# Kernel tuning notes

Measured on AMD Instinct MI355X. Metric: run time of the kernel, lower is better.

The kernel has to match this reference:

```python
import jax, jax.numpy as jnp
import numpy as np

TOKENS = 8192
HIDDEN = 4096
EPS = 1e-6
FP8_MAX = 448.0  # max finite value of float8_e4m3fn


def setup_inputs() -> dict:
    key = jax.random.key(0)
    k1, k2, k3 = jax.random.split(key, 3)
    x = jax.random.normal(k1, (TOKENS, HIDDEN), jnp.float32)
    # RMSNorm gains near 1
    norm_w = 1.0 + 0.1 * jax.random.normal(k2, (4, HIDDEN), jnp.float32)
    Ws = 0.02 * jax.random.normal(k3, (3, HIDDEN, HIDDEN), jnp.float32)
    # static per-tensor weight scales (amax / fp8_max)
    w_scales = jnp.max(jnp.abs(Ws), axis=(1, 2)) / FP8_MAX
    return {"x": x, "norm_w": norm_w, "Ws": Ws, "w_scales": w_scales}


def _rmsnorm(x, w):
    var = jnp.mean(x * x, axis=-1, keepdims=True)
    return x * jax.lax.rsqrt(var + EPS) * w


def _quant_dequant_fp8(v, s):
    # quantize to e4m3 with scale s, then dequantize (emulated fp8 GEMM inputs)
    q = (v / s).astype(jnp.float8_e4m3fn)
    return q.astype(jnp.float32) * s


def _fp8_linear(y, W, w_scale):
    # dynamic per-token activation scale
    a_scale = jnp.maximum(jnp.max(jnp.abs(y), axis=-1, keepdims=True) / FP8_MAX, 1e-12)
    yq = _quant_dequant_fp8(y, a_scale)           # [T, H]
    Wq = _quant_dequant_fp8(W, w_scale)           # [H, H]
    return yq @ Wq.T                              # torch.nn.Linear convention


def reference(x, norm_w, Ws, w_scales):
    x = jax.nn.relu(x)
    resid = x
    y = _rmsnorm(x, norm_w[0])                    # plain RMSNorm
    for i in range(3):
        h = _fp8_linear(y, Ws[i], w_scales[i])    # FP8 GEMM
        resid = h + resid                         # fused add + RMSNorm
        y = _rmsnorm(resid, norm_w[i + 1])
    return y
```

## Files before the change

### kernel.cpp

```cpp
#include <hip/hip_runtime.h>
#include <stdint.h>

#define TOKENS 8192
#define HIDDEN 4096
constexpr float EPS = 1e-6f;
constexpr float FP8_MAX = 448.0f;

using f32x4  = __attribute__((ext_vector_type(4))) float;
using f32x16 = __attribute__((ext_vector_type(16))) float;
using i32x4  = __attribute__((ext_vector_type(4))) int;
using i32x8  = __attribute__((ext_vector_type(8))) int;

typedef __attribute__((address_space(3))) uint32_t lds_u32_t;
typedef const __attribute__((address_space(1))) uint32_t glb_u32_t;

__device__ inline uint32_t pack_fp8x4(float a, float b, float c, float d) {
    int w = 0;
    w = __builtin_amdgcn_cvt_pk_fp8_f32(a, b, w, false);
    w = __builtin_amdgcn_cvt_pk_fp8_f32(c, d, w, true);
    return (uint32_t)w;
}

__device__ inline float block_sum(float v, float* sh, int tid) {
#pragma unroll
    for (int o = 32; o > 0; o >>= 1) v += __shfl_xor(v, o, 64);
    if ((tid & 63) == 0) sh[tid >> 6] = v;
    __syncthreads();
    return sh[0] + sh[1] + sh[2] + sh[3];
}
__device__ inline float block_max(float v, float* sh, int tid) {
#pragma unroll
    for (int o = 32; o > 0; o >>= 1) v = fmaxf(v, __shfl_xor(v, o, 64));
    if ((tid & 63) == 0) sh[tid >> 6] = v;
    __syncthreads();
    return fmaxf(fmaxf(sh[0], sh[1]), fmaxf(sh[2], sh[3]));
}

__launch_bounds__(256)
__global__ void quant_weights(const float* __restrict__ Ws,
                              const float* __restrict__ w_scales,
                              uint8_t* __restrict__ Wq) {
    size_t idx = ((size_t)blockIdx.x * 256 + threadIdx.x) * 8;
    int tensor = (int)(idx / ((size_t)HIDDEN * HIDDEN));
    float inv = 1.0f / w_scales[tensor];
    const float4* src = (const float4*)(Ws + idx);
    float4 v0 = src[0], v1 = src[1];
    uint2 out;
    out.x = pack_fp8x4(v0.x * inv, v0.y * inv, v0.z * inv, v0.w * inv);
    out.y = pack_fp8x4(v1.x * inv, v1.y * inv, v1.z * inv, v1.w * inv);
    *(uint2*)(Wq + idx) = out;
}

__launch_bounds__(256)
__global__ void relu_rms_quant(const float* __restrict__ x,
                               const float* __restrict__ nw,
                               float* __restrict__ resid,
                               uint8_t* __restrict__ yq,
                               float* __restrict__ ascale) {
    __shared__ float sh1[4], sh2[4];
    const int row = blockIdx.x, tid = threadIdx.x;
    const float* xr = x + (size_t)row * HIDDEN;
    float* rr = resid + (size_t)row * HIDDEN;

    float4 v[4];
    float ss = 0.f;
#pragma unroll
    for (int c = 0; c < 4; ++c) {
        float4 t = *(const float4*)(xr + c * 1024 + tid * 4);
        t.x = fmaxf(t.x, 0.f); t.y = fmaxf(t.y, 0.f);
        t.z = fmaxf(t.z, 0.f); t.w = fmaxf(t.w, 0.f);
        v[c] = t;
        ss += t.x * t.x + t.y * t.y + t.z * t.z + t.w * t.w;
        *(float4*)(rr + c * 1024 + tid * 4) = t;
    }
    ss = block_sum(ss, sh1, tid);
    float rstd = 1.0f / sqrtf(ss * (1.0f / HIDDEN) + EPS);

    float4 y[4];
    float amax = 0.f;
#pragma unroll
    for (int c = 0; c < 4; ++c) {
        float4 w = *(const float4*)(nw + c * 1024 + tid * 4);
        y[c].x = v[c].x * rstd * w.x; amax = fmaxf(amax, fabsf(y[c].x));
        y[c].y = v[c].y * rstd * w.y; amax = fmaxf(amax, fabsf(y[c].y));
        y[c].z = v[c].z * rstd * w.z; amax = fmaxf(amax, fabsf(y[c].z));
        y[c].w = v[c].w * rstd * w.w; amax = fmaxf(amax, fabsf(y[c].w));
    }
    amax = block_max(amax, sh2, tid);
    float s = fmaxf(amax / FP8_MAX, 1e-12f);
    if (tid == 0) ascale[row] = s;
    float inv = 1.0f / s;
#pragma unroll
    for (int c = 0; c < 4; ++c) {
        uint32_t p = pack_fp8x4(y[c].x * inv, y[c].y * inv, y[c].z * inv, y[c].w * inv);
        *(uint32_t*)(yq + (size_t)row * HIDDEN + c * 1024 + tid * 4) = p;
    }
}

__launch_bounds__(256)
__global__ void rms_quant(const float* __restrict__ resid,
                          const float* __restrict__ nw,
                          uint8_t* __restrict__ yq,
                          float* __restrict__ ascale) {
    __shared__ float sh1[4], sh2[4];
    const int row = blockIdx.x, tid = threadIdx.x;
    const float* rr = resid + (size_t)row * HIDDEN;

    float4 v[4];
    float ss = 0.f;
#pragma unroll
    for (int c = 0; c < 4; ++c) {
        float4 t = *(const float4*)(rr + c * 1024 + tid * 4);
        v[c] = t;
        ss += t.x * t.x + t.y * t.y + t.z * t.z + t.w * t.w;
    }
    ss = block_sum(ss, sh1, tid);
    float rstd = 1.0f / sqrtf(ss * (1.0f / HIDDEN) + EPS);

    float4 y[4];
    float amax = 0.f;
#pragma unroll
    for (int c = 0; c < 4; ++c) {
        float4 w = *(const float4*)(nw + c * 1024 + tid * 4);
        y[c].x = v[c].x * rstd * w.x; amax = fmaxf(amax, fabsf(y[c].x));
        y[c].y = v[c].y * rstd * w.y; amax = fmaxf(amax, fabsf(y[c].y));
        y[c].z = v[c].z * rstd * w.z; amax = fmaxf(amax, fabsf(y[c].z));
        y[c].w = v[c].w * rstd * w.w; amax = fmaxf(amax, fabsf(y[c].w));
    }
    amax = block_max(amax, sh2, tid);
    float s = fmaxf(amax / FP8_MAX, 1e-12f);
    if (tid == 0) ascale[row] = s;
    float inv = 1.0f / s;
#pragma unroll
    for (int c = 0; c < 4; ++c) {
        uint32_t p = pack_fp8x4(y[c].x * inv, y[c].y * inv, y[c].z * inv, y[c].w * inv);
        *(uint32_t*)(yq + (size_t)row * HIDDEN + c * 1024 + tid * 4) = p;
    }
}

__launch_bounds__(256)
__global__ void rms_final(const float* __restrict__ resid,
                          const float* __restrict__ nw,
                          float* __restrict__ out) {
    __shared__ float sh1[4];
    const int row = blockIdx.x, tid = threadIdx.x;
    const float* rr = resid + (size_t)row * HIDDEN;

    float4 v[4];
    float ss = 0.f;
#pragma unroll
    for (int c = 0; c < 4; ++c) {
        float4 t = *(const float4*)(rr + c * 1024 + tid * 4);
        v[c] = t;
        ss += t.x * t.x + t.y * t.y + t.z * t.z + t.w * t.w;
    }
    ss = block_sum(ss, sh1, tid);
    float rstd = 1.0f / sqrtf(ss * (1.0f / HIDDEN) + EPS);

#pragma unroll
    for (int c = 0; c < 4; ++c) {
        float4 w = *(const float4*)(nw + c * 1024 + tid * 4);
        float4 o;
        o.x = v[c].x * rstd * w.x;
        o.y = v[c].y * rstd * w.y;
        o.z = v[c].z * rstd * w.z;
        o.w = v[c].w * rstd * w.w;
        *(float4*)(out + (size_t)row * HIDDEN + c * 1024 + tid * 4) = o;
    }
}

#define BM 128
#define BN 128
#define BK 64

__launch_bounds__(256)
__global__ void gemm_fp8(const uint8_t* __restrict__ Aq,
                         const uint8_t* __restrict__ Bq,
                         const float* __restrict__ ascale,
                         const float* __restrict__ wscale_p,
                         float* __restrict__ resid) {
    __shared__ __align__(16) uint8_t sA[BM * BK];
    __shared__ __align__(16) uint8_t sB[BN * BK];
    __shared__ float s_as[BM];

    const int tid = threadIdx.x;
    int bid = blockIdx.x;
    bid = (bid & 7) * 256 + (bid >> 3);
    const int nbn = HIDDEN / BN;
    const int bm = bid / nbn, bn = bid % nbn;
    const int brow = bm * BM, bcol = bn * BN;

    const int wave = tid >> 6, lane = tid & 63;
    const int wm = wave >> 1, wn = wave & 1;
    const int lr = lane & 31;
    const int lh = lane >> 5;

    if (tid < BM) s_as[tid] = ascale[brow + tid];

    f32x16 acc[2][2] = {};

    const uint8_t* aSrc = Aq + (size_t)brow * HIDDEN;
    const uint8_t* bSrc = Bq + (size_t)bcol * HIDDEN;

    const int r_st = tid >> 2;
    const int g_st = tid & 3;
    const int gsrc = g_st ^ ((r_st >> 1) & 3);
    const size_t off0 = (size_t)r_st * HIDDEN + gsrc * 16;
    const size_t off1 = (size_t)(r_st + 64) * HIDDEN + gsrc * 16;
    uint8_t* ldsA0 = &sA[wave * 1024];
    uint8_t* ldsA1 = &sA[4096 + wave * 1024];
    uint8_t* ldsB0 = &sB[wave * 1024];
    uint8_t* ldsB1 = &sB[4096 + wave * 1024];

    int offA[2][2], offB[2][2];
#pragma unroll
    for (int m = 0; m < 2; ++m) {
        int ra = wm * 64 + m * 32 + lr;
        int sa_ = (ra >> 1) & 3;
        offA[m][0] = ra * 64 + ((2 * lh + 0) ^ sa_) * 16;
        offA[m][1] = ra * 64 + ((2 * lh + 1) ^ sa_) * 16;
        int rb = wn * 64 + m * 32 + lr;
        int sb_ = (rb >> 1) & 3;
        offB[m][0] = rb * 64 + ((2 * lh + 0) ^ sb_) * 16;
        offB[m][1] = rb * 64 + ((2 * lh + 1) ^ sb_) * 16;
    }

    const int UNIT = 0x7F7F7F7F;

    for (int k0 = 0; k0 < HIDDEN; k0 += BK) {
        __syncthreads();
        __builtin_amdgcn_global_load_lds((glb_u32_t*)(aSrc + off0 + k0),
                                         (lds_u32_t*)ldsA0, 16, 0, 0);
        __builtin_amdgcn_global_load_lds((glb_u32_t*)(aSrc + off1 + k0),
                                         (lds_u32_t*)ldsA1, 16, 0, 0);
        __builtin_amdgcn_global_load_lds((glb_u32_t*)(bSrc + off0 + k0),
                                         (lds_u32_t*)ldsB0, 16, 0, 0);
        __builtin_amdgcn_global_load_lds((glb_u32_t*)(bSrc + off1 + k0),
                                         (lds_u32_t*)ldsB1, 16, 0, 0);
        __syncthreads();

        i32x8 a[2], b[2];
#pragma unroll
        for (int m = 0; m < 2; ++m) {
            i32x4 lo = *(const i32x4*)&sA[offA[m][0]];
            i32x4 hi = *(const i32x4*)&sA[offA[m][1]];
            a[m] = __builtin_shufflevector(lo, hi, 0, 1, 2, 3, 4, 5, 6, 7);
        }
#pragma unroll
        for (int n = 0; n < 2; ++n) {
            i32x4 lo = *(const i32x4*)&sB[offB[n][0]];
            i32x4 hi = *(const i32x4*)&sB[offB[n][1]];
            b[n] = __builtin_shufflevector(lo, hi, 0, 1, 2, 3, 4, 5, 6, 7);
        }
#pragma unroll
        for (int m = 0; m < 2; ++m)
#pragma unroll
            for (int n = 0; n < 2; ++n)
                acc[m][n] = __builtin_amdgcn_mfma_scale_f32_32x32x64_f8f6f4(
                    a[m], b[n], acc[m][n], 0, 0, 0, UNIT, 0, UNIT);
    }

    const float wsc = *wscale_p;
#pragma unroll
    for (int m = 0; m < 2; ++m)
#pragma unroll
        for (int n = 0; n < 2; ++n) {
            const int col = bcol + wn * 64 + n * 32 + lr;
#pragma unroll
            for (int i = 0; i < 16; ++i) {
                const int rl = (i & 3) + 8 * (i >> 2) + 4 * lh;
                const int row_local = wm * 64 + m * 32 + rl;
                const float alpha = s_as[row_local] * wsc;
                const size_t o = (size_t)(brow + row_local) * HIDDEN + col;
                resid[o] += acc[m][n][i] * alpha;
            }
        }
}

extern "C" void kernel_launch(void* const* d_in, const int* in_sizes, int n_in,
                              void* d_out, int out_size, void* d_ws, size_t ws_size,
                              hipStream_t stream) {
    const float* x   = (const float*)d_in[0];
    const float* nw  = (const float*)d_in[1];
    const float* Ws  = (const float*)d_in[2];
    const float* wsc = (const float*)d_in[3];
    float* out = (float*)d_out;

    uint8_t* ws = (uint8_t*)d_ws;
    float*   resid  = (float*)ws;
    uint8_t* yq     = ws + (size_t)TOKENS * HIDDEN * 4;
    uint8_t* Wq     = yq + (size_t)TOKENS * HIDDEN;
    float*   ascale = (float*)(Wq + (size_t)3 * HIDDEN * HIDDEN);

    quant_weights<<<(3 * (size_t)HIDDEN * HIDDEN) / 2048, 256, 0, stream>>>(Ws, wsc, Wq);

    relu_rms_quant<<<TOKENS, 256, 0, stream>>>(x, nw, resid, yq, ascale);

    for (int i = 0; i < 3; ++i) {
        gemm_fp8<<<(TOKENS / BM) * (HIDDEN / BN), 256, 0, stream>>>(
            yq, Wq + (size_t)i * HIDDEN * HIDDEN, ascale, wsc + i, resid);
        if (i < 2)
            rms_quant<<<TOKENS, 256, 0, stream>>>(resid, nw + (size_t)(i + 1) * HIDDEN, yq, ascale);
        else
            rms_final<<<TOKENS, 256, 0, stream>>>(resid, nw + (size_t)3 * HIDDEN, out);
    }
}
```

Measured before the change: 810.4 us.

## Double-buffer LDS tiles in FP8 GEMM to overlap loads with MFMA

```diff
diff --git a/kernel.cpp b/kernel.cpp
--- a/kernel.cpp
+++ b/kernel.cpp
@@ -179,8 +179,8 @@
                          const float* __restrict__ ascale,
                          const float* __restrict__ wscale_p,
                          float* __restrict__ resid) {
-    __shared__ __align__(16) uint8_t sA[BM * BK];
-    __shared__ __align__(16) uint8_t sB[BN * BK];
+    __shared__ __align__(16) uint8_t sA[2][BM * BK];
+    __shared__ __align__(16) uint8_t sB[2][BN * BK];
     __shared__ float s_as[BM];
 
     const int tid = threadIdx.x;
@@ -207,10 +207,8 @@
     const int gsrc = g_st ^ ((r_st >> 1) & 3);
     const size_t off0 = (size_t)r_st * HIDDEN + gsrc * 16;
     const size_t off1 = (size_t)(r_st + 64) * HIDDEN + gsrc * 16;
-    uint8_t* ldsA0 = &sA[wave * 1024];
-    uint8_t* ldsA1 = &sA[4096 + wave * 1024];
-    uint8_t* ldsB0 = &sB[wave * 1024];
-    uint8_t* ldsB1 = &sB[4096 + wave * 1024];
+    const int lds0 = wave * 1024;
+    const int lds1 = 4096 + wave * 1024;
 
     int offA[2][2], offB[2][2];
 #pragma unroll
@@ -227,29 +225,28 @@
 
     const int UNIT = 0x7F7F7F7F;
 
-    for (int k0 = 0; k0 < HIDDEN; k0 += BK) {
-        __syncthreads();
+    auto stage = [&](int buf, int k0) {
         __builtin_amdgcn_global_load_lds((glb_u32_t*)(aSrc + off0 + k0),
-                                         (lds_u32_t*)ldsA0, 16, 0, 0);
+                                         (lds_u32_t*)&sA[buf][lds0], 16, 0, 0);
         __builtin_amdgcn_global_load_lds((glb_u32_t*)(aSrc + off1 + k0),
-                                         (lds_u32_t*)ldsA1, 16, 0, 0);
+                                         (lds_u32_t*)&sA[buf][lds1], 16, 0, 0);
         __builtin_amdgcn_global_load_lds((glb_u32_t*)(bSrc + off0 + k0),
-                                         (lds_u32_t*)ldsB0, 16, 0, 0);
+                                         (lds_u32_t*)&sB[buf][lds0], 16, 0, 0);
         __builtin_amdgcn_global_load_lds((glb_u32_t*)(bSrc + off1 + k0),
-                                         (lds_u32_t*)ldsB1, 16, 0, 0);
-        __syncthreads();
-
+                                         (lds_u32_t*)&sB[buf][lds1], 16, 0, 0);
+    };
+    auto compute = [&](int buf) {
         i32x8 a[2], b[2];
 #pragma unroll
         for (int m = 0; m < 2; ++m) {
-            i32x4 lo = *(const i32x4*)&sA[offA[m][0]];
-            i32x4 hi = *(const i32x4*)&sA[offA[m][1]];
+            i32x4 lo = *(const i32x4*)&sA[buf][offA[m][0]];
+            i32x4 hi = *(const i32x4*)&sA[buf][offA[m][1]];
             a[m] = __builtin_shufflevector(lo, hi, 0, 1, 2, 3, 4, 5, 6, 7);
         }
 #pragma unroll
         for (int n = 0; n < 2; ++n) {
-            i32x4 lo = *(const i32x4*)&sB[offB[n][0]];
-            i32x4 hi = *(const i32x4*)&sB[offB[n][1]];
+            i32x4 lo = *(const i32x4*)&sB[buf][offB[n][0]];
+            i32x4 hi = *(const i32x4*)&sB[buf][offB[n][1]];
             b[n] = __builtin_shufflevector(lo, hi, 0, 1, 2, 3, 4, 5, 6, 7);
         }
 #pragma unroll
@@ -258,6 +255,19 @@
             for (int n = 0; n < 2; ++n)
                 acc[m][n] = __builtin_amdgcn_mfma_scale_f32_32x32x64_f8f6f4(
                     a[m], b[n], acc[m][n], 0, 0, 0, UNIT, 0, UNIT);
+    };
+
+    stage(0, 0);
+    __syncthreads();
+
+    const int NT = HIDDEN / BK;
+    for (int t = 0; t < NT; t += 2) {
+        stage(1, (t + 1) * BK);
+        compute(0);
+        __syncthreads();
+        if (t + 2 < NT) stage(0, (t + 2) * BK);
+        compute(1);
+        __syncthreads();
     }
 
     const float wsc = *wscale_p;
```

Result: faster. 788.6 us (-2.7%).
